# Performance work log

Hardware: AMD Instinct MI355X
Metric: run time of the kernel (lower is better)

Reference implementation:

```python
import jax, jax.numpy as jnp
import numpy as np

EMBED_DIM = 1024
NUM_HEADS = 16
TGT_LEN = 2048
SRC_LEN = 2048
BSZ = 8
SCALING = float(EMBED_DIM // NUM_HEADS) ** (-0.5)


def setup_inputs() -> dict:
    key = jax.random.key(0)
    k1, k2, k3, k4 = jax.random.split(key, 4)
    q1 = jax.random.normal(k1, (TGT_LEN, BSZ, EMBED_DIM), dtype=jnp.float32)
    k = jax.random.normal(k2, (SRC_LEN, BSZ, EMBED_DIM), dtype=jnp.float32)
    value = jax.random.normal(k3, (SRC_LEN, BSZ, EMBED_DIM), dtype=jnp.float32)
    # nn.Linear weight [out, in], xavier-ish scale
    W = jax.random.normal(k4, (EMBED_DIM, EMBED_DIM), dtype=jnp.float32) / np.sqrt(EMBED_DIM)
    b = jnp.zeros((EMBED_DIM,), dtype=jnp.float32)
    return {"q1": q1, "k": k, "value": value, "W": W, "b": b}


def reference(q1, k, value, W, b):
    # q1: [T, B, E], k: [S, B, E]; `value` is unused (module projects v from k).
    del value
    v = k @ W.T + b                      # [S, B, E] fused v-projection
    q = (q1 * SCALING).transpose(1, 0, 2)  # [B, T, E]
    kt = k.transpose(1, 0, 2)              # [B, S, E]
    vt = v.transpose(1, 0, 2)              # [B, S, E]
    scores = jnp.einsum('bte,bse->bts', q, kt)   # [B, T, S]
    attn = jax.nn.softmax(scores, axis=-1)
    out = jnp.einsum('bts,bse->bte', attn, vt)   # [B, T, E]
    return out.transpose(1, 0, 2)                # [T, B, E]
```

## Files before the change

### kernel.cpp

```cpp
#include <hip/hip_runtime.h>
#include <hip/hip_bf16.h>

#define E_DIM 1024
#define T_LEN 2048
#define S_LEN 2048
#define B_SZ  8
#define SCALE 0.125f

typedef short short8 __attribute__((ext_vector_type(8)));
typedef float f32x4 __attribute__((ext_vector_type(4)));

#define BARRIER() __builtin_amdgcn_s_barrier()

static __device__ __forceinline__ unsigned short f2bf(float f) {
  __hip_bfloat16 h = __float2bfloat16(f);
  return __builtin_bit_cast(unsigned short, h);
}

__global__ __launch_bounds__(256) void prep_kernel(
    const float* __restrict__ q1, const float* __restrict__ kin,
    const float* __restrict__ W,
    unsigned short* __restrict__ qbf, unsigned short* __restrict__ kbf,
    unsigned short* __restrict__ wbf, float* __restrict__ denom) {
  const int QV = B_SZ * T_LEN * (E_DIM / 4);
  const int WV = (E_DIM * E_DIM) / 4;
  const int DN = (B_SZ * T_LEN) / 4;
  const int total = 2 * QV + WV + DN;
  for (int idx = blockIdx.x * blockDim.x + threadIdx.x; idx < total;
       idx += gridDim.x * blockDim.x) {
    if (idx < QV) {
      int e4 = idx & 255;
      int bt = idx >> 8;
      int t = bt & (T_LEN - 1);
      int b = bt >> 11;
      float4 v = reinterpret_cast<const float4*>(q1)[(t * B_SZ + b) * 256 + e4];
      ushort4 o;
      o.x = f2bf(v.x * SCALE); o.y = f2bf(v.y * SCALE);
      o.z = f2bf(v.z * SCALE); o.w = f2bf(v.w * SCALE);
      reinterpret_cast<ushort4*>(qbf)[idx] = o;
    } else if (idx < 2 * QV) {
      int d = idx - QV;
      int e4 = d & 255;
      int bt = d >> 8;
      int s = bt & (T_LEN - 1);
      int b = bt >> 11;
      float4 v = reinterpret_cast<const float4*>(kin)[(s * B_SZ + b) * 256 + e4];
      ushort4 o;
      o.x = f2bf(v.x); o.y = f2bf(v.y); o.z = f2bf(v.z); o.w = f2bf(v.w);
      reinterpret_cast<ushort4*>(kbf)[d] = o;
    } else if (idx < 2 * QV + WV) {
      int d = idx - 2 * QV;
      float4 v = reinterpret_cast<const float4*>(W)[d];
      ushort4 o;
      o.x = f2bf(v.x); o.y = f2bf(v.y); o.z = f2bf(v.z); o.w = f2bf(v.w);
      reinterpret_cast<ushort4*>(wbf)[d] = o;
    } else {
      int d = idx - 2 * QV - WV;
      float4 z; z.x = z.y = z.z = z.w = 0.f;
      reinterpret_cast<float4*>(denom)[d] = z;
    }
  }
}

#define RD(ptr, off) (*reinterpret_cast<const short8*>((ptr) + (off)))

#define STAGE(srcs, dstBase, KOFF)                                            \
  {                                                                           \
    _Pragma("unroll") for (int p_ = 0; p_ < 2; ++p_) {                        \
      unsigned short* dst_ = (dstBase) + (size_t)(p_ * 512 + wave * 64) * 8;  \
      __builtin_amdgcn_global_load_lds(                                       \
          (const __attribute__((address_space(1))) unsigned int*)             \
              ((srcs)[p_] + (KOFF)),                                          \
          (__attribute__((address_space(3))) unsigned int*)dst_, 16, 0, 0);   \
    }                                                                         \
  }

#define MFMAQ(MB, NB, AF, BF)                                                 \
  {                                                                           \
    _Pragma("unroll") for (int m_ = 0; m_ < 4; ++m_)                          \
      _Pragma("unroll") for (int n_ = 0; n_ < 2; ++n_)                        \
        _Pragma("unroll") for (int ks_ = 0; ks_ < 2; ++ks_)                   \
          acc[MB + m_][NB + n_] = __builtin_amdgcn_mfma_f32_16x16x32_bf16(    \
              AF[m_][ks_], BF[n_][ks_], acc[MB + m_][NB + n_], 0, 0, 0);      \
  }

#define KTILE(S, DO_B, DO_A, KOB, KOA)                                        \
  {                                                                           \
                     \
    if (DO_B) STAGE(sB, ldsB + (1 - S) * 16384, KOB);                         \
    _Pragma("unroll") for (int m = 0; m < 4; ++m) {                           \
      aH[m][0] = RD(pA0, S * 16384 + (4 + m) * 1024);                         \
      aH[m][1] = RD(pA1, S * 16384 + (4 + m) * 1024);                         \
    }                                                                         \
    __builtin_amdgcn_s_setprio(1);                                            \
    MFMAQ(0, 0, aL, b01);                                                     \
    __builtin_amdgcn_s_setprio(0);                                            \
    BARRIER();                                                        \
                    \
    if (DO_B) STAGE(sB, ldsB + (1 - S) * 16384 + 8192, (KOB) + HB);           \
    _Pragma("unroll") for (int n = 0; n < 2; ++n) {                           \
      b23[n][0] = RD(pB0, S * 16384 + (2 + n) * 1024);                        \
      b23[n][1] = RD(pB1, S * 16384 + (2 + n) * 1024);                        \
    }                                                                         \
    __builtin_amdgcn_s_setprio(1);                                            \
    MFMAQ(4, 0, aH, b01);                                                     \
    __builtin_amdgcn_s_setprio(0);                                            \
    BARRIER();                                                        \
                                   \
    if (DO_A) STAGE(sA, ldsA + S * 16384, KOA);                               \
    __builtin_amdgcn_s_setprio(1);                                            \
    MFMAQ(0, 2, aL, b23);                                                     \
    __builtin_amdgcn_s_setprio(0);                                            \
    BARRIER();                                                        \
       \
    if (DO_A) {                                                               \
      STAGE(sA, ldsA + S * 16384 + 8192, (KOA) + HA);                         \
      asm volatile("s_waitcnt vmcnt(4)" ::: "memory");                        \
    } else {                                                                  \
      asm volatile("s_waitcnt vmcnt(0)" ::: "memory");                        \
    }                                                                         \
    BARRIER();                     \
    _Pragma("unroll") for (int m = 0; m < 4; ++m) {                           \
      aL[m][0] = RD(pA0, (1 - S) * 16384 + m * 1024);                         \
      aL[m][1] = RD(pA1, (1 - S) * 16384 + m * 1024);                         \
    }                                                                         \
    _Pragma("unroll") for (int n = 0; n < 2; ++n) {                           \
      b01[n][0] = RD(pB0, (1 - S) * 16384 + n * 1024);                        \
      b01[n][1] = RD(pB1, (1 - S) * 16384 + n * 1024);                        \
    }                                                                         \
    __builtin_amdgcn_s_setprio(1);                                            \
    MFMAQ(4, 2, aH, b23);                                                     \
    __builtin_amdgcn_s_setprio(0);                                            \
    BARRIER();                                        \
  }

__device__ __forceinline__ void gemm256(
    const unsigned short* __restrict__ A, size_t lda, int r0,
    const unsigned short* __restrict__ B, size_t ldb, int c0,
    int NKT, unsigned short* lds, f32x4 acc[8][4]) {
  const int tid = threadIdx.x;
  const int lane = tid & 63, wave = tid >> 6;
  const int lr = lane & 15, lg = lane >> 4;
  const int wr = wave >> 2, wc = wave & 3;
  unsigned short* ldsA = lds;
  unsigned short* ldsB = lds + 4 * 8192;
  const size_t HA = 128 * lda;
  const size_t HB = 128 * ldb;

  const unsigned short* pA0 = ldsA + wr * 8192 + lr * 64 + ((0 + lg) ^ (lr & 7)) * 8;
  const unsigned short* pA1 = ldsA + wr * 8192 + lr * 64 + ((4 + lg) ^ (lr & 7)) * 8;
  const unsigned short* pB0 = ldsB + (wc >> 1) * 8192 + ((wc & 1) * 64 + lr) * 64 +
                              ((0 + lg) ^ (lr & 7)) * 8;
  const unsigned short* pB1 = ldsB + (wc >> 1) * 8192 + ((wc & 1) * 64 + lr) * 64 +
                              ((4 + lg) ^ (lr & 7)) * 8;

  const unsigned short* sA[2]; const unsigned short* sB[2];
#pragma unroll
  for (int p = 0; p < 2; ++p) {
    int c = p * 512 + tid, row = c >> 3, cg = (c & 7) ^ (row & 7);
    sA[p] = A + (size_t)(r0 + row) * lda + cg * 8;
    sB[p] = B + (size_t)(c0 + row) * ldb + cg * 8;
  }

  short8 aL[4][2], aH[4][2], b01[2][2], b23[2][2];

  STAGE(sA, ldsA, 0);
  STAGE(sA, ldsA + 8192, HA);
  STAGE(sB, ldsB, 0);
  STAGE(sB, ldsB + 8192, HB);
  STAGE(sA, ldsA + 16384, 64);
  STAGE(sA, ldsA + 16384 + 8192, HA + 64);
  asm volatile("s_waitcnt vmcnt(4)" ::: "memory");
  BARRIER();
#pragma unroll
  for (int m = 0; m < 4; ++m) {
    aL[m][0] = RD(pA0, m * 1024);
    aL[m][1] = RD(pA1, m * 1024);
  }
#pragma unroll
  for (int n = 0; n < 2; ++n) {
    b01[n][0] = RD(pB0, n * 1024);
    b01[n][1] = RD(pB1, n * 1024);
  }

  const int nit = NKT >> 1;
  for (int it = 0; it < nit; ++it) {
    const bool notLast = (it != nit - 1);
    KTILE(0, true, notLast, 64, 128);
    KTILE(1, notLast, notLast, 128, 192);
#pragma unroll
    for (int p = 0; p < 2; ++p) { sA[p] += 128; sB[p] += 128; }
  }
}

__global__ __launch_bounds__(512, 2) void proj_kernel(
    const unsigned short* __restrict__ kbf,
    const unsigned short* __restrict__ wbf,
    const float* __restrict__ bias,
    unsigned short* __restrict__ vT) {
  __shared__ unsigned short lds[65536];
  const int lane = threadIdx.x & 63, wave = threadIdx.x >> 6;
  const int lr = lane & 15, lg = lane >> 4;
  const int wr = wave >> 2, wc = wave & 3;
  const int r0 = blockIdx.x * 256;
  const int c0 = blockIdx.y * 256;
  f32x4 acc[8][4] = {};
  gemm256(kbf, E_DIM, r0, wbf, E_DIM, c0, E_DIM / 64, lds, acc);
#pragma unroll
  for (int n = 0; n < 4; ++n) {
    int o = c0 + wc * 64 + n * 16 + lr;
    float bv = bias[o];
#pragma unroll
    for (int m = 0; m < 8; ++m) {
#pragma unroll
      for (int i = 0; i < 4; ++i) {
        int r = r0 + wr * 128 + m * 16 + lg * 4 + i;
        int b = r >> 11;
        int s = r & (S_LEN - 1);
        vT[((size_t)b * E_DIM + o) * S_LEN + s] = f2bf(acc[m][n][i] + bv);
      }
    }
  }
}

__global__ __launch_bounds__(512, 2) void scores_kernel(
    const unsigned short* __restrict__ qbf,
    const unsigned short* __restrict__ kbf,
    unsigned short* __restrict__ P, float* __restrict__ denom,
    int tbase, int trows, int ntx) {
  __shared__ unsigned short lds[65536];
  const int nwg = gridDim.x;
  const int per = nwg >> 3;
  const int wgid = (blockIdx.x & 7) * per + (blockIdx.x >> 3);
  const int b = wgid / (ntx * 8);
  const int rem = wgid - b * (ntx * 8);
  const int ty = rem / ntx;
  const int tx = rem - ty * ntx;
  const int lane = threadIdx.x & 63, wave = threadIdx.x >> 6;
  const int lr = lane & 15, lg = lane >> 4;
  const int wr = wave >> 2, wc = wave & 3;
  const int t0l = tx * 256;
  const int s0 = ty * 256;
  const unsigned short* Q = qbf + (size_t)b * T_LEN * E_DIM;
  const unsigned short* K = kbf + (size_t)b * S_LEN * E_DIM;
  f32x4 acc[8][4] = {};
  gemm256(Q, E_DIM, tbase + t0l, K, E_DIM, s0, E_DIM / 64, lds, acc);
  unsigned short* outp = P + (size_t)b * trows * S_LEN;
  float* dn = denom + (size_t)b * T_LEN + tbase;
#pragma unroll
  for (int m = 0; m < 8; ++m) {
#pragma unroll
    for (int i = 0; i < 4; ++i) {
      int tl = t0l + wr * 128 + m * 16 + lg * 4 + i;
      float rp = 0.f;
#pragma unroll
      for (int n = 0; n < 4; ++n) {
        float e = __expf(acc[m][n][i]);
        rp += e;
        int s = s0 + wc * 64 + n * 16 + lr;
        outp[(size_t)tl * S_LEN + s] = f2bf(e);
      }
#pragma unroll
      for (int off = 1; off < 16; off <<= 1) rp += __shfl_xor(rp, off);
      if (lr == 0) atomicAdd(&dn[tl], rp);
    }
  }
}

__global__ __launch_bounds__(512, 2) void pv_kernel(
    const unsigned short* __restrict__ pbf,
    const unsigned short* __restrict__ vT,
    const float* __restrict__ denom,
    float* __restrict__ out, int tbase, int trows, int ntx) {
  __shared__ unsigned short lds[65536];
  const int nwg = gridDim.x;
  const int per = nwg >> 3;
  const int wgid = (blockIdx.x & 7) * per + (blockIdx.x >> 3);
  const int b = wgid / (ntx * 4);
  const int rem = wgid - b * (ntx * 4);
  const int ey = rem / ntx;
  const int tx = rem - ey * ntx;
  const int lane = threadIdx.x & 63, wave = threadIdx.x >> 6;
  const int lr = lane & 15, lg = lane >> 4;
  const int wr = wave >> 2, wc = wave & 3;
  const int tl0 = tx * 256;
  const int e0 = ey * 256;
  const unsigned short* Pp = pbf + (size_t)b * trows * S_LEN;
  const unsigned short* V = vT + (size_t)b * E_DIM * S_LEN;
  f32x4 acc[8][4] = {};
  gemm256(Pp, S_LEN, tl0, V, S_LEN, e0, S_LEN / 64, lds, acc);
  const float* dn = denom + (size_t)b * T_LEN + tbase;
#pragma unroll
  for (int m = 0; m < 8; ++m) {
#pragma unroll
    for (int i = 0; i < 4; ++i) {
      int tl = tl0 + wr * 128 + m * 16 + lg * 4 + i;
      float invd = 1.0f / dn[tl];
      int t = tbase + tl;
#pragma unroll
      for (int n = 0; n < 4; ++n) {
        int e = e0 + wc * 64 + n * 16 + lr;
        out[((size_t)t * B_SZ + b) * E_DIM + e] = acc[m][n][i] * invd;
      }
    }
  }
}

extern "C" void kernel_launch(void* const* d_in, const int* in_sizes, int n_in,
                              void* d_out, int out_size, void* d_ws, size_t ws_size,
                              hipStream_t stream) {
  const float* q1 = (const float*)d_in[0];
  const float* k = (const float*)d_in[1];
  const float* W = (const float*)d_in[3];
  const float* bias = (const float*)d_in[4];
  float* out = (float*)d_out;

  char* ws = (char*)d_ws;
  const size_t QB = (size_t)B_SZ * T_LEN * E_DIM * 2;
  const size_t WBYTES = (size_t)E_DIM * E_DIM * 2;
  const size_t DBYTES = (size_t)B_SZ * T_LEN * 4;
  unsigned short* qbf = (unsigned short*)(ws);
  unsigned short* kbf = (unsigned short*)(ws + QB);
  unsigned short* vT = (unsigned short*)(ws + 2 * QB);
  unsigned short* wbf = (unsigned short*)(ws + 3 * QB);
  float* denom = (float*)(ws + 3 * QB + WBYTES);
  unsigned short* P = (unsigned short*)(ws + 3 * QB + WBYTES + DBYTES);
  const size_t fixed = 3 * QB + WBYTES + DBYTES;

  size_t avail = ws_size > fixed ? ws_size - fixed : 0;
  int tpc = (int)(avail / ((size_t)B_SZ * S_LEN * 2));
  tpc = (tpc / 256) * 256;
  if (tpc > T_LEN) tpc = T_LEN;
  if (tpc < 256) tpc = 256;

  prep_kernel<<<dim3(2048), dim3(256), 0, stream>>>(q1, k, W, qbf, kbf, wbf,
                                                    denom);
  proj_kernel<<<dim3((B_SZ * S_LEN) / 256, E_DIM / 256), dim3(512), 0, stream>>>(
      kbf, wbf, bias, vT);

  for (int tbase = 0; tbase < T_LEN; tbase += tpc) {
    int trows = T_LEN - tbase < tpc ? T_LEN - tbase : tpc;
    int ntx = trows / 256;
    scores_kernel<<<dim3(ntx * (S_LEN / 256) * B_SZ), dim3(512), 0, stream>>>(
        qbf, kbf, P, denom, tbase, trows, ntx);
    pv_kernel<<<dim3(ntx * (E_DIM / 256) * B_SZ), dim3(512), 0, stream>>>(
        P, vT, denom, out, tbase, trows, ntx);
  }
}
```

Measured before the change: 225.4 us.

## Switch GEMM core to 32x32x16 bf16 MFMA with restructured LDS pipeline

Replaces the 16x16x32 MFMA tiling in the shared 256x256 GEMM with 32x32x16 MFMA instructions. Accumulators become 4x2 f32x16 per wave, with new swizzled LDS read pointers and per-quarter fragment loads. The k-tile schedule adds extra barriers and lgkmcnt(0) waits, and fragments are no longer prefetched across k-tiles. Epilogues for the V-projection, scores and PV kernels are remapped, and the V-projection now writes vectorized 4-element stores. The larger MFMA is meant to cut instruction issue and LDS read traffic per FLOP, at the cost of less LDS/MFMA overlap from the added synchronization.

```diff
diff --git a/kernel.cpp b/kernel.cpp
--- a/kernel.cpp
+++ b/kernel.cpp
@@ -8,7 +8,8 @@
 #define SCALE 0.125f
 
 typedef short short8 __attribute__((ext_vector_type(8)));
-typedef float f32x4 __attribute__((ext_vector_type(4)));
+typedef float f32x16 __attribute__((ext_vector_type(16)));
+typedef unsigned short ushort4v __attribute__((ext_vector_type(4)));
 
 #define BARRIER() __builtin_amdgcn_s_barrier()
 
@@ -75,84 +76,89 @@
     }                                                                         \
   }
 
-#define MFMAQ(MB, NB, AF, BF)                                                 \
+#define MFMAQ32(MB, N, AF, BF)                                                \
   {                                                                           \
-    _Pragma("unroll") for (int m_ = 0; m_ < 4; ++m_)                          \
-      _Pragma("unroll") for (int n_ = 0; n_ < 2; ++n_)                        \
-        _Pragma("unroll") for (int ks_ = 0; ks_ < 2; ++ks_)                   \
-          acc[MB + m_][NB + n_] = __builtin_amdgcn_mfma_f32_16x16x32_bf16(    \
-              AF[m_][ks_], BF[n_][ks_], acc[MB + m_][NB + n_], 0, 0, 0);      \
-  }
+    _Pragma("unroll") for (int mm_ = 0; mm_ < 2; ++mm_)                       \
+      _Pragma("unroll") for (int ks_ = 0; ks_ < 4; ++ks_)                     \
+        acc[MB + mm_][N] = __builtin_amdgcn_mfma_f32_32x32x16_bf16(           \
+            AF[mm_][ks_], BF[ks_], acc[MB + mm_][N], 0, 0, 0);                \
+  }
+
+#define LGKM0() asm volatile("s_waitcnt lgkmcnt(0)" ::: "memory")
 
 #define KTILE(S, DO_B, DO_A, KOB, KOA)                                        \
   {                                                                           \
+    short8 aLo[2][4], aHi[2][4], b0[4], b1[4];                                \
+            \
+    _Pragma("unroll") for (int mm = 0; mm < 2; ++mm)                          \
+      _Pragma("unroll") for (int ks = 0; ks < 4; ++ks)                        \
+        aLo[mm][ks] = RD(pAk[ks], S * 16384 + mm * 2048);                     \
+    _Pragma("unroll") for (int ks = 0; ks < 4; ++ks)                          \
+      b0[ks] = RD(pBk[ks], S * 16384);                                        \
+    if (DO_B) STAGE(sB, ldsB + (1 - S) * 16384, KOB);                         \
+    BARRIER();                                                                \
+    __builtin_amdgcn_s_setprio(1);                                            \
+    MFMAQ32(0, 0, aLo, b0);                                                   \
+    __builtin_amdgcn_s_setprio(0);                                            \
+    LGKM0();                                                                  \
+    BARRIER();                                                                \
                      \
-    if (DO_B) STAGE(sB, ldsB + (1 - S) * 16384, KOB);                         \
-    _Pragma("unroll") for (int m = 0; m < 4; ++m) {                           \
-      aH[m][0] = RD(pA0, S * 16384 + (4 + m) * 1024);                         \
-      aH[m][1] = RD(pA1, S * 16384 + (4 + m) * 1024);                         \
-    }                                                                         \
+    _Pragma("unroll") for (int mm = 0; mm < 2; ++mm)                          \
+      _Pragma("unroll") for (int ks = 0; ks < 4; ++ks)                        \
+        aHi[mm][ks] = RD(pAk[ks], S * 16384 + (2 + mm) * 2048);               \
+    if (DO_B) STAGE(sB, ldsB + (1 - S) * 16384 + 8192, (KOB) + HB);           \
+    BARRIER();                                                                \
     __builtin_amdgcn_s_setprio(1);                                            \
-    MFMAQ(0, 0, aL, b01);                                                     \
+    MFMAQ32(2, 0, aHi, b0);                                                   \
     __builtin_amdgcn_s_setprio(0);                                            \
-    BARRIER();                                                        \
-                    \
-    if (DO_B) STAGE(sB, ldsB + (1 - S) * 16384 + 8192, (KOB) + HB);           \
-    _Pragma("unroll") for (int n = 0; n < 2; ++n) {                           \
-      b23[n][0] = RD(pB0, S * 16384 + (2 + n) * 1024);                        \
-      b23[n][1] = RD(pB1, S * 16384 + (2 + n) * 1024);                        \
-    }                                                                         \
+    LGKM0();                                                                  \
+    BARRIER();                                                                \
+                        \
+    _Pragma("unroll") for (int ks = 0; ks < 4; ++ks)                          \
+      b1[ks] = RD(pBk[ks], S * 16384 + 2048);                                 \
+    if (DO_A) STAGE(sA, ldsA + S * 16384, KOA);                               \
+    BARRIER();                                                                \
     __builtin_amdgcn_s_setprio(1);                                            \
-    MFMAQ(4, 0, aH, b01);                                                     \
+    MFMAQ32(0, 1, aLo, b1);                                                   \
     __builtin_amdgcn_s_setprio(0);                                            \
-    BARRIER();                                                        \
-                                   \
-    if (DO_A) STAGE(sA, ldsA + S * 16384, KOA);                               \
-    __builtin_amdgcn_s_setprio(1);                                            \
-    MFMAQ(0, 2, aL, b23);                                                     \
-    __builtin_amdgcn_s_setprio(0);                                            \
-    BARRIER();                                                        \
-       \
+    LGKM0();                                                                  \
+    BARRIER();                                                                \
+                      \
     if (DO_A) {                                                               \
       STAGE(sA, ldsA + S * 16384 + 8192, (KOA) + HA);                         \
       asm volatile("s_waitcnt vmcnt(4)" ::: "memory");                        \
     } else {                                                                  \
       asm volatile("s_waitcnt vmcnt(0)" ::: "memory");                        \
     }                                                                         \
-    BARRIER();                     \
-    _Pragma("unroll") for (int m = 0; m < 4; ++m) {                           \
-      aL[m][0] = RD(pA0, (1 - S) * 16384 + m * 1024);                         \
-      aL[m][1] = RD(pA1, (1 - S) * 16384 + m * 1024);                         \
-    }                                                                         \
-    _Pragma("unroll") for (int n = 0; n < 2; ++n) {                           \
-      b01[n][0] = RD(pB0, (1 - S) * 16384 + n * 1024);                        \
-      b01[n][1] = RD(pB1, (1 - S) * 16384 + n * 1024);                        \
-    }                                                                         \
+    BARRIER();                                                                \
     __builtin_amdgcn_s_setprio(1);                                            \
-    MFMAQ(4, 2, aH, b23);                                                     \
+    MFMAQ32(2, 1, aHi, b1);                                                   \
     __builtin_amdgcn_s_setprio(0);                                            \
-    BARRIER();                                        \
+    LGKM0();                                                                  \
+    BARRIER();                                                                \
   }
 
 __device__ __forceinline__ void gemm256(
     const unsigned short* __restrict__ A, size_t lda, int r0,
     const unsigned short* __restrict__ B, size_t ldb, int c0,
-    int NKT, unsigned short* lds, f32x4 acc[8][4]) {
+    int NKT, unsigned short* lds, f32x16 acc[4][2]) {
   const int tid = threadIdx.x;
   const int lane = tid & 63, wave = tid >> 6;
-  const int lr = lane & 15, lg = lane >> 4;
+  const int l31 = lane & 31, hi = lane >> 5;
   const int wr = wave >> 2, wc = wave & 3;
   unsigned short* ldsA = lds;
   unsigned short* ldsB = lds + 4 * 8192;
   const size_t HA = 128 * lda;
   const size_t HB = 128 * ldb;
 
-  const unsigned short* pA0 = ldsA + wr * 8192 + lr * 64 + ((0 + lg) ^ (lr & 7)) * 8;
-  const unsigned short* pA1 = ldsA + wr * 8192 + lr * 64 + ((4 + lg) ^ (lr & 7)) * 8;
-  const unsigned short* pB0 = ldsB + (wc >> 1) * 8192 + ((wc & 1) * 64 + lr) * 64 +
-                              ((0 + lg) ^ (lr & 7)) * 8;
-  const unsigned short* pB1 = ldsB + (wc >> 1) * 8192 + ((wc & 1) * 64 + lr) * 64 +
-                              ((4 + lg) ^ (lr & 7)) * 8;
+  const unsigned short* pAk[4];
+  const unsigned short* pBk[4];
+#pragma unroll
+  for (int ks = 0; ks < 4; ++ks) {
+    int ch = (ks * 2 + hi) ^ (lane & 7);
+    pAk[ks] = ldsA + wr * 8192 + l31 * 64 + ch * 8;
+    pBk[ks] = ldsB + (wc >> 1) * 8192 + ((wc & 1) * 64 + l31) * 64 + ch * 8;
+  }
 
   const unsigned short* sA[2]; const unsigned short* sB[2];
 #pragma unroll
@@ -161,8 +167,6 @@
     sA[p] = A + (size_t)(r0 + row) * lda + cg * 8;
     sB[p] = B + (size_t)(c0 + row) * ldb + cg * 8;
   }
-
-  short8 aL[4][2], aH[4][2], b01[2][2], b23[2][2];
 
   STAGE(sA, ldsA, 0);
   STAGE(sA, ldsA + 8192, HA);
@@ -172,16 +176,6 @@
   STAGE(sA, ldsA + 16384 + 8192, HA + 64);
   asm volatile("s_waitcnt vmcnt(4)" ::: "memory");
   BARRIER();
-#pragma unroll
-  for (int m = 0; m < 4; ++m) {
-    aL[m][0] = RD(pA0, m * 1024);
-    aL[m][1] = RD(pA1, m * 1024);
-  }
-#pragma unroll
-  for (int n = 0; n < 2; ++n) {
-    b01[n][0] = RD(pB0, n * 1024);
-    b01[n][1] = RD(pB1, n * 1024);
-  }
 
   const int nit = NKT >> 1;
   for (int it = 0; it < nit; ++it) {
@@ -200,24 +194,29 @@
     unsigned short* __restrict__ vT) {
   __shared__ unsigned short lds[65536];
   const int lane = threadIdx.x & 63, wave = threadIdx.x >> 6;
-  const int lr = lane & 15, lg = lane >> 4;
+  const int l31 = lane & 31, hi = lane >> 5;
   const int wr = wave >> 2, wc = wave & 3;
   const int r0 = blockIdx.x * 256;
   const int c0 = blockIdx.y * 256;
-  f32x4 acc[8][4] = {};
+  f32x16 acc[4][2] = {};
   gemm256(kbf, E_DIM, r0, wbf, E_DIM, c0, E_DIM / 64, lds, acc);
-#pragma unroll
-  for (int n = 0; n < 4; ++n) {
-    int o = c0 + wc * 64 + n * 16 + lr;
+
+  const int bb = r0 >> 11;
+  const int sbase = r0 & (S_LEN - 1);
+#pragma unroll
+  for (int n = 0; n < 2; ++n) {
+    int o = c0 + wc * 64 + n * 32 + l31;
     float bv = bias[o];
-#pragma unroll
-    for (int m = 0; m < 8; ++m) {
-#pragma unroll
-      for (int i = 0; i < 4; ++i) {
-        int r = r0 + wr * 128 + m * 16 + lg * 4 + i;
-        int b = r >> 11;
-        int s = r & (S_LEN - 1);
-        vT[((size_t)b * E_DIM + o) * S_LEN + s] = f2bf(acc[m][n][i] + bv);
+    unsigned short* orow = vT + ((size_t)bb * E_DIM + o) * S_LEN + sbase;
+#pragma unroll
+    for (int m = 0; m < 4; ++m) {
+#pragma unroll
+      for (int q = 0; q < 4; ++q) {
+        ushort4v w;
+#pragma unroll
+        for (int i = 0; i < 4; ++i) w[i] = f2bf(acc[m][n][q * 4 + i] + bv);
+        *reinterpret_cast<ushort4v*>(orow + wr * 128 + m * 32 + q * 8 + 4 * hi)
+            = w;
       }
     }
   }
@@ -237,32 +236,30 @@
   const int ty = rem / ntx;
   const int tx = rem - ty * ntx;
   const int lane = threadIdx.x & 63, wave = threadIdx.x >> 6;
-  const int lr = lane & 15, lg = lane >> 4;
+  const int l31 = lane & 31, hi = lane >> 5;
   const int wr = wave >> 2, wc = wave & 3;
   const int t0l = tx * 256;
   const int s0 = ty * 256;
   const unsigned short* Q = qbf + (size_t)b * T_LEN * E_DIM;
   const unsigned short* K = kbf + (size_t)b * S_LEN * E_DIM;
-  f32x4 acc[8][4] = {};
+  f32x16 acc[4][2] = {};
   gemm256(Q, E_DIM, tbase + t0l, K, E_DIM, s0, E_DIM / 64, lds, acc);
   unsigned short* outp = P + (size_t)b * trows * S_LEN;
   float* dn = denom + (size_t)b * T_LEN + tbase;
-#pragma unroll
-  for (int m = 0; m < 8; ++m) {
-#pragma unroll
-    for (int i = 0; i < 4; ++i) {
-      int tl = t0l + wr * 128 + m * 16 + lg * 4 + i;
-      float rp = 0.f;
-#pragma unroll
-      for (int n = 0; n < 4; ++n) {
-        float e = __expf(acc[m][n][i]);
-        rp += e;
-        int s = s0 + wc * 64 + n * 16 + lr;
-        outp[(size_t)tl * S_LEN + s] = f2bf(e);
-      }
-#pragma unroll
-      for (int off = 1; off < 16; off <<= 1) rp += __shfl_xor(rp, off);
-      if (lr == 0) atomicAdd(&dn[tl], rp);
+  const int scol = s0 + wc * 64 + l31;
+#pragma unroll
+  for (int m = 0; m < 4; ++m) {
+#pragma unroll
+    for (int r = 0; r < 16; ++r) {
+      int tl = t0l + wr * 128 + m * 32 + (r & 3) + 8 * (r >> 2) + 4 * hi;
+      float e0 = __expf(acc[m][0][r]);
+      float e1 = __expf(acc[m][1][r]);
+      outp[(size_t)tl * S_LEN + scol] = f2bf(e0);
+      outp[(size_t)tl * S_LEN + scol + 32] = f2bf(e1);
+      float rp = e0 + e1;
+#pragma unroll
+      for (int off = 1; off < 32; off <<= 1) rp += __shfl_xor(rp, off);
+      if (l31 == 0) atomicAdd(&dn[tl], rp);
     }
   }
 }
@@ -281,27 +278,26 @@
   const int ey = rem / ntx;
   const int tx = rem - ey * ntx;
   const int lane = threadIdx.x & 63, wave = threadIdx.x >> 6;
-  const int lr = lane & 15, lg = lane >> 4;
+  const int l31 = lane & 31, hi = lane >> 5;
   const int wr = wave >> 2, wc = wave & 3;
   const int tl0 = tx * 256;
   const int e0 = ey * 256;
   const unsigned short* Pp = pbf + (size_t)b * trows * S_LEN;
   const unsigned short* V = vT + (size_t)b * E_DIM * S_LEN;
-  f32x4 acc[8][4] = {};
+  f32x16 acc[4][2] = {};
   gemm256(Pp, S_LEN, tl0, V, S_LEN, e0, S_LEN / 64, lds, acc);
   const float* dn = denom + (size_t)b * T_LEN + tbase;
-#pragma unroll
-  for (int m = 0; m < 8; ++m) {
-#pragma unroll
-    for (int i = 0; i < 4; ++i) {
-      int tl = tl0 + wr * 128 + m * 16 + lg * 4 + i;
+  const int ecol = e0 + wc * 64 + l31;
+#pragma unroll
+  for (int m = 0; m < 4; ++m) {
+#pragma unroll
+    for (int r = 0; r < 16; ++r) {
+      int tl = tl0 + wr * 128 + m * 32 + (r & 3) + 8 * (r >> 2) + 4 * hi;
       float invd = 1.0f / dn[tl];
       int t = tbase + tl;
-#pragma unroll
-      for (int n = 0; n < 4; ++n) {
-        int e = e0 + wc * 64 + n * 16 + lr;
-        out[((size_t)t * B_SZ + b) * E_DIM + e] = acc[m][n][i] * invd;
-      }
+      float* orow = out + ((size_t)t * B_SZ + b) * E_DIM;
+      orow[ecol] = acc[m][0][r] * invd;
+      orow[ecol + 32] = acc[m][1][r] * invd;
     }
   }
 }
```

Result: slower. 248.5 us (+10.3%).
